# Kernel optimization log

Measured on AMD Instinct MI355X. Metric: run time of the kernel, lower is better.

Reference implementation:

```python
import jax, jax.numpy as jnp
import numpy as np

N_USERS = 60000
N_ITEMS = 40000
N_NODES = N_USERS + N_ITEMS  # 100000
N_EDGES = 3_200_000
EMB_DIM = 64
N_LAYERS = 3
S_TEMP = 1.0  # config['s_temp']
EPS = 1e-16   # torch_geometric.utils.softmax denominator eps


def segment_softmax(logits, seg, num_segments):
    # numerically stable scatter-softmax (PyG softmax semantics)
    m = jax.ops.segment_max(logits, seg, num_segments=num_segments)
    m = jnp.where(jnp.isfinite(m), m, 0.0)  # empty segments -> -inf guard
    e = jnp.exp(logits - m[seg])
    s = jax.ops.segment_sum(e, seg, num_segments=num_segments)
    return e / (s[seg] + EPS)


def setup_inputs() -> dict:
    key = jax.random.key(0)
    k1, k2, k3 = jax.random.split(key, 3)
    # nn.Embedding weight, init normal(std=0.1) for non-NGCF models
    emb = jax.random.normal(k1, (N_NODES, EMB_DIM), dtype=jnp.float32) * 0.1
    edge_index = jax.random.randint(k2, (2, N_EDGES), 0, N_NODES, dtype=jnp.int32)
    edge_attrs = jax.random.normal(k3, (N_EDGES,), dtype=jnp.float32)
    return {"emb": emb, "edge_index": edge_index, "edge_attrs": edge_attrs}


def reference(emb, edge_index, edge_attrs):
    from_, to_ = edge_index[0], edge_index[1]
    logits = edge_attrs / S_TEMP
    incoming = segment_softmax(logits, to_, N_NODES)
    outgoing = segment_softmax(logits, from_, N_NODES)
    norm = jnp.sqrt(incoming * outgoing)  # abl_study == 0 branch

    embs = [emb]
    cur = emb
    for _ in range(N_LAYERS):
        # message: norm * x_j ; aggregate: scatter-add at to_
        msg = norm[:, None] * cur[from_]           # [E, D]
        cur = jax.ops.segment_sum(msg, to_, num_segments=N_NODES)  # [N, D]
        embs.append(cur)

    out = jnp.mean(jnp.stack(embs, axis=0), axis=0)  # lightGCN-style layer mean
    return (emb, out)
```

## Files before the change

kernel.cpp:

```cpp
#include <hip/hip_runtime.h>
#include <math.h>
#include <hip/hip_fp16.h>

#define N_NODES 100000
#define N_EDGES 3200000
#define EPS 1e-16f
#define BSH 8
#define BN 256
#define NBK 391
#define PTT 512
#define PE2 8
#define PTILE (PTT * PE2)
#define GR (PTILE / 16)
#define PBLOCKS ((N_EDGES + PTILE - 1) / PTILE)
#define CAP 9216u
#define NR 4
#define SCALE 8.0f
#define RPT 9

typedef float    f4v __attribute__((ext_vector_type(4)));
typedef float    f2v __attribute__((ext_vector_type(2)));

static __device__ __forceinline__ float4 nt_load_f4(const float4* p) {
    f4v v = __builtin_nontemporal_load((const f4v*)p);
    return make_float4(v.x, v.y, v.z, v.w);
}
static __device__ __forceinline__ int range_of(unsigned f) {
    return (f >= 50000u) ? (f >= 75000u ? 3 : 2) : (f >= 25000u ? 1 : 0);
}

static __device__ __forceinline__ unsigned short f_to_bf(float f) {
    unsigned u = __float_as_uint(f);
    unsigned r = (u + 0x7FFFu + ((u >> 16) & 1u)) >> 16;
    return (unsigned short)r;
}
static __device__ __forceinline__ float slot_w(unsigned s) {
    return __half2float(__ushort_as_half((unsigned short)(s >> 17)));
}
static __device__ __forceinline__ void fma8_fp8(float w, uint2 r, float* a) {
    f2v v0 = __builtin_amdgcn_cvt_pk_f32_fp8((int)r.x, false);
    f2v v1 = __builtin_amdgcn_cvt_pk_f32_fp8((int)r.x, true);
    f2v v2 = __builtin_amdgcn_cvt_pk_f32_fp8((int)r.y, false);
    f2v v3 = __builtin_amdgcn_cvt_pk_f32_fp8((int)r.y, true);
    a[0] = fmaf(w, v0.x, a[0]); a[1] = fmaf(w, v0.y, a[1]);
    a[2] = fmaf(w, v1.x, a[2]); a[3] = fmaf(w, v1.y, a[3]);
    a[4] = fmaf(w, v2.x, a[4]); a[5] = fmaf(w, v2.y, a[5]);
    a[6] = fmaf(w, v3.x, a[6]); a[7] = fmaf(w, v3.y, a[7]);
}
static __device__ __forceinline__ uint4 pack8(const float* a) {
    uint4 o;
    o.x = (unsigned)f_to_bf(a[0]) | ((unsigned)f_to_bf(a[1]) << 16);
    o.y = (unsigned)f_to_bf(a[2]) | ((unsigned)f_to_bf(a[3]) << 16);
    o.z = (unsigned)f_to_bf(a[4]) | ((unsigned)f_to_bf(a[5]) << 16);
    o.w = (unsigned)f_to_bf(a[6]) | ((unsigned)f_to_bf(a[7]) << 16);
    return o;
}
static __device__ __forceinline__ uint2 pack8_fp8(const float* a) {
    int w0 = __builtin_amdgcn_cvt_pk_fp8_f32(a[0], a[1], 0, false);
    w0 = __builtin_amdgcn_cvt_pk_fp8_f32(a[2], a[3], w0, true);
    int w1 = __builtin_amdgcn_cvt_pk_fp8_f32(a[4], a[5], 0, false);
    w1 = __builtin_amdgcn_cvt_pk_fp8_f32(a[6], a[7], w1, true);
    return make_uint2((unsigned)w0, (unsigned)w1);
}
static __device__ __forceinline__ float bfu_to_f(unsigned u, int hi) {
    return __uint_as_float(hi ? (u & 0xFFFF0000u) : (u << 16));
}

__global__ __launch_bounds__(PTT) void partition(
        const int* __restrict__ ei, const float* __restrict__ attr,
        unsigned* __restrict__ pos_t, unsigned* __restrict__ pos_f,
        uint2* __restrict__ bt, unsigned* __restrict__ bf) {
    __shared__ unsigned ht[NBK], hf[NBK];
    __shared__ unsigned hbt[NBK + 1], hbf[NBK + 1];
    __shared__ unsigned dlt[NBK], dlf[NBK];
    __shared__ unsigned short lutT[GR], lutF[GR];
    __shared__ unsigned wsum[8];
    __shared__ unsigned sbtx[PTILE];
    __shared__ unsigned short sbty[PTILE];
    __shared__ unsigned sbf[PTILE];
    const int tid = threadIdx.x;
    const int lane = tid & 63, wid = tid >> 6;
    for (int i = tid; i < NBK; i += PTT) { ht[i] = 0; hf[i] = 0; }
    __syncthreads();
    const int tile = blockIdx.x * PTILE;
    const int tcount = (tile + PTILE < N_EDGES) ? PTILE : (N_EDGES - tile);
    unsigned fv[PE2], tv[PE2];
    unsigned short xh[PE2];
    #pragma unroll
    for (int k = 0; k < PE2; ++k) {
        int e = tile + k * PTT + tid;
        if (e < N_EDGES) {
            fv[k] = (unsigned)__builtin_nontemporal_load(&ei[e]);
            tv[k] = (unsigned)__builtin_nontemporal_load(&ei[N_EDGES + e]);
            xh[k] = __half_as_ushort(__float2half(
                        __expf(__builtin_nontemporal_load(&attr[e]))));
            atomicAdd(&ht[tv[k] >> BSH], 1u);
            atomicAdd(&hf[fv[k] >> BSH], 1u);
        } else {
            tv[k] = 0xFFFFFFFFu;
        }
    }
    __syncthreads();
    unsigned ot = (tid < NBK) ? ht[tid] : 0u;
    unsigned of = (tid < NBK) ? hf[tid] : 0u;
    unsigned own = ot | (of << 16);
    unsigned x = own;
    #pragma unroll
    for (int d = 1; d < 64; d <<= 1) {
        unsigned v = __shfl_up(x, d, 64);
        if (lane >= d) x += v;
    }
    if (lane == 63) wsum[wid] = x;
    __syncthreads();
    unsigned pre = 0;
    for (int w = 0; w < wid; ++w) pre += wsum[w];
    unsigned excl = x + pre - own;
    unsigned et = excl & 0xFFFFu, ef = excl >> 16;
    if (tid < NBK) {
        hbt[tid] = et;
        hbf[tid] = ef;
        unsigned rt = ot ? atomicAdd(&pos_t[tid], ot) : 0u;
        unsigned rf = of ? atomicAdd(&pos_f[tid], of) : 0u;
        dlt[tid] = tid * CAP + rt - et;
        dlf[tid] = tid * CAP + rf - ef;
    }
    if (tid == NBK - 1) { hbt[NBK] = et + ot; hbf[NBK] = ef + of; }
    __syncthreads();
    if (tid < NBK) {
        unsigned b0 = hbt[tid], b1 = hbt[tid + 1];
        for (unsigned g = (b0 + 15u) >> 4; (g << 4) < b1; ++g) lutT[g] = (unsigned short)tid;
        b0 = hbf[tid]; b1 = hbf[tid + 1];
        for (unsigned g = (b0 + 15u) >> 4; (g << 4) < b1; ++g) lutF[g] = (unsigned short)tid;
    }
    for (int i = tid; i < NBK; i += PTT) { ht[i] = hbt[i]; hf[i] = hbf[i]; }
    __syncthreads();
    #pragma unroll
    for (int k = 0; k < PE2; ++k) {
        if (tv[k] != 0xFFFFFFFFu) {
            unsigned p = atomicAdd(&ht[tv[k] >> BSH], 1u);
            sbtx[p] = fv[k] | ((tv[k] & (BN - 1u)) << 17);
            sbty[p] = xh[k];
            unsigned q = atomicAdd(&hf[fv[k] >> BSH], 1u);
            sbf[q] = ((fv[k] & (BN - 1u)) << 16) | (unsigned)xh[k];
        }
    }
    __syncthreads();
    for (int i = tid; i < tcount; i += PTT) {
        unsigned b = lutT[i >> 4];
        while (hbt[b + 1] <= (unsigned)i) ++b;
        unsigned ga = dlt[b] + (unsigned)i;
        if (ga < (b + 1u) * CAP) bt[ga] = make_uint2(sbtx[i], (unsigned)sbty[i]);
    }
    for (int i = tid; i < tcount; i += PTT) {
        unsigned b = lutF[i >> 4];
        while (hbf[b + 1] <= (unsigned)i) ++b;
        unsigned ga = dlf[b] + (unsigned)i;
        if (ga < (b + 1u) * CAP) bf[ga] = sbf[i];
    }
}

__global__ __launch_bounds__(1024) void bucket_build(
        const unsigned* __restrict__ pos_f, const unsigned* __restrict__ bf,
        const unsigned* __restrict__ pos_t, const uint2* __restrict__ bt,
        const float4* __restrict__ emb4, uint2* __restrict__ emb_f8,
        uint2* __restrict__ row2, unsigned* __restrict__ slots,
        float2* __restrict__ sc2) {
    __shared__ float s[BN];
    __shared__ float sto[BN];
    __shared__ unsigned cnt[BN][NR];
    __shared__ unsigned cur[BN][NR];
    __shared__ unsigned wsum[4];
    int b = blockIdx.x, tid = threadIdx.x;
    const int lane = tid & 63, wid = tid >> 6;
    if (tid < BN) {
        s[tid] = 0.f;
        sto[tid] = 0.f;
        #pragma unroll
        for (int r = 0; r < NR; ++r) cnt[tid][r] = 0;
    }
    __syncthreads();
    {
        unsigned fill = pos_f[b]; if (fill > CAP) fill = CAP;
        unsigned lof = b * CAP, hif = lof + fill;
        for (unsigned i = lof + tid; i < hif; i += 1024) {
            unsigned u = __builtin_nontemporal_load(&bf[i]);
            atomicAdd(&s[u >> 16], __half2float(__ushort_as_half((unsigned short)(u & 0xFFFFu))));
        }
    }
    __syncthreads();
    {
        int nl = tid >> 2, part = tid & 3;
        int node = b * BN + nl;
        if (node < N_NODES) {
            float rsv = rsqrtf(s[nl] + EPS) * SCALE;
            size_t rbase = (size_t)node * 16 + part * 4;
            #pragma unroll
            for (int c = 0; c < 2; ++c) {
                float4 v0 = emb4[rbase + c * 2];
                float4 v1 = emb4[rbase + c * 2 + 1];
                float a[8] = {v0.x * rsv, v0.y * rsv, v0.z * rsv, v0.w * rsv,
                              v1.x * rsv, v1.y * rsv, v1.z * rsv, v1.w * rsv};
                emb_f8[(size_t)node * 8 + part * 2 + c] = pack8_fp8(a);
            }
        }
    }
    unsigned fill = pos_t[b]; if (fill > CAP) fill = CAP;
    unsigned lo = b * CAP, hi = lo + fill;
    uint2 rv[RPT];
    #pragma unroll
    for (int j = 0; j < RPT; ++j) {
        unsigned i = lo + tid + (unsigned)j * 1024u;
        if (i < hi) {
            uint2 u = bt[i];
            rv[j] = u;
            unsigned tl = u.x >> 17;
            atomicAdd(&cnt[tl][range_of(u.x & 0x1FFFFu)], 1u);
            atomicAdd(&sto[tl], __half2float(__ushort_as_half((unsigned short)u.y)));
        } else {
            rv[j].x = 0xFFFFFFFFu;
            rv[j].y = 0u;
        }
    }
    __syncthreads();
    unsigned c0 = 0, c1 = 0, c2 = 0, c3 = 0, own = 0;
    if (tid < BN) {
        c0 = cnt[tid][0]; c1 = cnt[tid][1]; c2 = cnt[tid][2]; c3 = cnt[tid][3];
        own = c0 + c1 + c2 + c3;
    }
    unsigned x = own;
    #pragma unroll
    for (int d = 1; d < 64; d <<= 1) {
        unsigned v = __shfl_up(x, d, 64);
        if (lane >= d) x += v;
    }
    if (tid < BN && lane == 63) wsum[wid] = x;
    __syncthreads();
    if (tid < BN) {
        unsigned pre = 0;
        for (int w = 0; w < wid; ++w) pre += wsum[w];
        unsigned base = lo + x + pre - own;
        int node = b * BN + tid;
        if (node < N_NODES) {
            row2[node] = make_uint2(base, base + own);
            float rt = rsqrtf(sto[tid] + EPS);
            sc2[node] = make_float2(rt * (1.0f / SCALE), rt * rsqrtf(s[tid] + EPS));
        }
        cur[tid][0] = base;
        cur[tid][1] = base + c0;
        cur[tid][2] = base + c0 + c1;
        cur[tid][3] = base + c0 + c1 + c2;
    }
    __syncthreads();
    #pragma unroll
    for (int j = 0; j < RPT; ++j) {
        if (rv[j].x != 0xFFFFFFFFu) {
            unsigned tl = rv[j].x >> 17;
            unsigned f = rv[j].x & 0x1FFFFu;
            unsigned p = atomicAdd(&cur[tl][range_of(f)], 1u);
            slots[p] = f | (rv[j].y << 17);
        }
    }
}

#define GATHER_CORE8(TABLE)                                                       \
    float a[8] = {0, 0, 0, 0, 0, 0, 0, 0};                                        \
    float bacc[8] = {0, 0, 0, 0, 0, 0, 0, 0};                                     \
    unsigned k = beg;                                                             \
    for (; k + 8 <= end; k += 8) {                                                \
        unsigned s0 = slots[k], s1 = slots[k + 1], s2 = slots[k + 2], s3 = slots[k + 3]; \
        unsigned s4 = slots[k + 4], s5 = slots[k + 5], s6 = slots[k + 6], s7 = slots[k + 7]; \
        uint2 r0 = TABLE[(size_t)(s0 & 0x1FFFFu) * 8 + lane];                     \
        uint2 r1 = TABLE[(size_t)(s1 & 0x1FFFFu) * 8 + lane];                     \
        uint2 r2 = TABLE[(size_t)(s2 & 0x1FFFFu) * 8 + lane];                     \
        uint2 r3 = TABLE[(size_t)(s3 & 0x1FFFFu) * 8 + lane];                     \
        uint2 r4 = TABLE[(size_t)(s4 & 0x1FFFFu) * 8 + lane];                     \
        uint2 r5 = TABLE[(size_t)(s5 & 0x1FFFFu) * 8 + lane];                     \
        uint2 r6 = TABLE[(size_t)(s6 & 0x1FFFFu) * 8 + lane];                     \
        uint2 r7 = TABLE[(size_t)(s7 & 0x1FFFFu) * 8 + lane];                     \
        fma8_fp8(slot_w(s0), r0, a);    fma8_fp8(slot_w(s1), r1, bacc);           \
        fma8_fp8(slot_w(s2), r2, a);    fma8_fp8(slot_w(s3), r3, bacc);           \
        fma8_fp8(slot_w(s4), r4, a);    fma8_fp8(slot_w(s5), r5, bacc);           \
        fma8_fp8(slot_w(s6), r6, a);    fma8_fp8(slot_w(s7), r7, bacc);           \
    }                                                                             \
    for (; k < end; ++k) {                                                        \
        unsigned s = slots[k];                                                    \
        uint2 r = TABLE[(size_t)(s & 0x1FFFFu) * 8 + lane];                       \
        fma8_fp8(slot_w(s), r, a);                                                \
    }                                                                             \
    _Pragma("unroll")                                                             \
    for (int j = 0; j < 8; ++j) a[j] += bacc[j];

__global__ void prop1(const uint2* __restrict__ row2, const unsigned* __restrict__ slots,
                      const uint2* __restrict__ emb_f8, const float2* __restrict__ sc2,
                      uint2* __restrict__ T1f8, uint4* __restrict__ T1bf,
                      const float4* __restrict__ emb4, float4* __restrict__ out_emb4) {
    int node = blockIdx.x * 32 + (threadIdx.x >> 3);
    int lane = threadIdx.x & 7;
    if (node < N_NODES) {
        uint2 rp = row2[node];
        unsigned beg = rp.x, end = rp.y;
        GATHER_CORE8(emb_f8)
        float2 sc = sc2[node];
        float own[8], tab[8];
        #pragma unroll
        for (int j = 0; j < 8; ++j) { own[j] = a[j] * sc.x; tab[j] = a[j] * sc.y; }
        size_t o = (size_t)node * 8 + lane;
        T1bf[o] = pack8(own);
        T1f8[o] = pack8_fp8(tab);
    }
    const int total = N_NODES * 16;
    const int stride = ((N_NODES * 8 + 255) / 256) * 256;
    for (int i = blockIdx.x * 256 + threadIdx.x; i < total; i += stride) {
        out_emb4[i] = nt_load_f4(&emb4[i]);
    }
}

__global__ void prop2(const uint2* __restrict__ row2, const unsigned* __restrict__ slots,
                      const uint2* __restrict__ T1f8, const float2* __restrict__ sc2,
                      uint2* __restrict__ T2f8, uint4* __restrict__ T2bf) {
    int node = blockIdx.x * 32 + (threadIdx.x >> 3);
    int lane = threadIdx.x & 7;
    if (node >= N_NODES) return;
    uint2 rp = row2[node];
    unsigned beg = rp.x, end = rp.y;
    GATHER_CORE8(T1f8)
    float2 sc = sc2[node];
    float own[8], tab[8];
    #pragma unroll
    for (int j = 0; j < 8; ++j) { own[j] = a[j] * sc.x; tab[j] = a[j] * sc.y; }
    size_t o = (size_t)node * 8 + lane;
    T2bf[o] = pack8(own);
    T2f8[o] = pack8_fp8(tab);
}

__global__ void prop3(const uint2* __restrict__ row2, const unsigned* __restrict__ slots,
                      const uint2* __restrict__ T2f8, const float2* __restrict__ sc2,
                      const uint4* __restrict__ T1bf, const uint4* __restrict__ T2bf,
                      const float4* __restrict__ emb4, float4* __restrict__ acc) {
    int node = blockIdx.x * 32 + (threadIdx.x >> 3);
    int lane = threadIdx.x & 7;
    if (node >= N_NODES) return;
    uint2 rp = row2[node];
    unsigned beg = rp.x, end = rp.y;
    GATHER_CORE8(T2f8)
    float osc = sc2[node].x;
    size_t o = (size_t)node * 8 + lane;
    uint4 t1 = T1bf[o];
    uint4 t2 = T2bf[o];
    unsigned tw1[4] = {t1.x, t1.y, t1.z, t1.w};
    unsigned tw2[4] = {t2.x, t2.y, t2.z, t2.w};
    size_t o4 = (size_t)node * 16 + lane * 2;
    float4 e0 = emb4[o4], e1 = emb4[o4 + 1];
    float e[8] = {e0.x, e0.y, e0.z, e0.w, e1.x, e1.y, e1.z, e1.w};
    float r[8];
    #pragma unroll
    for (int j = 0; j < 8; ++j) {
        float l1v = bfu_to_f(tw1[j >> 1], j & 1);
        float l2v = bfu_to_f(tw2[j >> 1], j & 1);
        r[j] = (e[j] + l1v + l2v + a[j] * osc) * 0.25f;
    }
    acc[o4]     = make_float4(r[0], r[1], r[2], r[3]);
    acc[o4 + 1] = make_float4(r[4], r[5], r[6], r[7]);
}

extern "C" void kernel_launch(void* const* d_in, const int* in_sizes, int n_in,
                              void* d_out, int out_size, void* d_ws, size_t ws_size,
                              hipStream_t stream) {
    const float* emb = (const float*)d_in[0];
    const int* ei = (const int*)d_in[1];
    const float* attr = (const float*)d_in[2];

    float* out_emb = (float*)d_out;
    float* out_acc = out_emb + (size_t)N_NODES * 64;

    char* ws = (char*)d_ws;
    size_t off = 0;
    auto alloc = [&](size_t bytes) -> void* {
        void* p = ws + off;
        off += (bytes + 255) & ~(size_t)255;
        return p;
    };
    unsigned* pos_t   = (unsigned*)alloc((size_t)NBK * 4);
    unsigned* pos_f   = (unsigned*)alloc((size_t)NBK * 4);
    size_t zero_bytes = off;
    uint2*    row2    = (uint2*)   alloc((size_t)N_NODES * 8);
    float2*   sc2     = (float2*)  alloc((size_t)N_NODES * 8);
    uint2* bt         = (uint2*)   alloc((size_t)NBK * CAP * 8);
    unsigned* bfa     = (unsigned*)alloc((size_t)NBK * CAP * 4);
    unsigned* slots   = bfa;
    uint2* emb_f8     = (uint2*)   alloc((size_t)N_NODES * 64);
    uint2* T1f8       = (uint2*)   alloc((size_t)N_NODES * 64);
    uint4* T1bf       = (uint4*)   alloc((size_t)N_NODES * 128);
    uint2* T2f8 = (uint2*)bt;
    uint4* T2bf = (uint4*)((char*)bt + (size_t)N_NODES * 64);
    (void)ws_size;

    hipMemsetAsync(d_ws, 0, zero_bytes, stream);

    partition<<<PBLOCKS, PTT, 0, stream>>>(ei, attr, pos_t, pos_f, bt, bfa);
    bucket_build<<<NBK, 1024, 0, stream>>>(pos_f, bfa, pos_t, bt,
                                           (const float4*)emb, emb_f8,
                                           row2, slots, sc2);

    const int pgrid = (N_NODES * 8 + 255) / 256;
    prop1<<<pgrid, 256, 0, stream>>>(row2, slots, emb_f8, sc2, T1f8, T1bf,
                                     (const float4*)emb, (float4*)out_emb);
    prop2<<<pgrid, 256, 0, stream>>>(row2, slots, T1f8, sc2, T2f8, T2bf);
    prop3<<<pgrid, 256, 0, stream>>>(row2, slots, T2f8, sc2, T1bf, T2bf,
                                     (const float4*)emb, (float4*)out_acc);
}
```

Measured before the change: 247.7 us.

## Split bucket_build into from-sum and to-CSR kernels; separate load and atomic loops

Splits the fused bucket_build kernel into two launches. bucket_sum_f computes per-source softmax denominators and the fp8 embedding table. bucket_csr_t builds the CSR slots by re-reading the bt bucket in a second pass instead of holding 9 uint2 entries per thread in registers. In partition, the global loads are hoisted into their own loop ahead of the LDS histogram atomics so more loads can be in flight. This trades an extra launch, an extra global read of bt, and a small s_from_inv buffer for lower register pressure and possibly better occupancy and load overlap.

```diff
diff --git a/kernel.cpp b/kernel.cpp
--- a/kernel.cpp
+++ b/kernel.cpp
@@ -16,7 +16,6 @@
 #define CAP 9216u
 #define NR 4
 #define SCALE 8.0f
-#define RPT 9
 
 typedef float    f4v __attribute__((ext_vector_type(4)));
 typedef float    f2v __attribute__((ext_vector_type(2)));
@@ -94,10 +93,15 @@
             tv[k] = (unsigned)__builtin_nontemporal_load(&ei[N_EDGES + e]);
             xh[k] = __half_as_ushort(__float2half(
                         __expf(__builtin_nontemporal_load(&attr[e]))));
+        } else {
+            tv[k] = 0xFFFFFFFFu;
+        }
+    }
+    #pragma unroll
+    for (int k = 0; k < PE2; ++k) {
+        if (tv[k] != 0xFFFFFFFFu) {
             atomicAdd(&ht[tv[k] >> BSH], 1u);
             atomicAdd(&hf[fv[k] >> BSH], 1u);
-        } else {
-            tv[k] = 0xFFFFFFFFu;
         }
     }
     __syncthreads();
@@ -159,13 +163,46 @@
     }
 }
 
-__global__ __launch_bounds__(1024) void bucket_build(
+__global__ __launch_bounds__(1024) void bucket_sum_f(
         const unsigned* __restrict__ pos_f, const unsigned* __restrict__ bf,
+        float* __restrict__ s_from_inv,
+        const float4* __restrict__ emb4, uint2* __restrict__ emb_f8) {
+    __shared__ float s[BN];
+    int b = blockIdx.x, tid = threadIdx.x;
+    if (tid < BN) s[tid] = 0.f;
+    __syncthreads();
+    unsigned fill = pos_f[b]; if (fill > CAP) fill = CAP;
+    unsigned lo = b * CAP, hi = lo + fill;
+    for (unsigned i = lo + tid; i < hi; i += 1024) {
+        unsigned u = __builtin_nontemporal_load(&bf[i]);
+        atomicAdd(&s[u >> 16], __half2float(__ushort_as_half((unsigned short)(u & 0xFFFFu))));
+    }
+    __syncthreads();
+    if (tid < BN) {
+        int node = b * BN + tid;
+        if (node < N_NODES) s_from_inv[node] = rsqrtf(s[tid] + EPS);
+    }
+    int nl = tid >> 2, part = tid & 3;
+    int node = b * BN + nl;
+    if (node < N_NODES) {
+        float rsv = rsqrtf(s[nl] + EPS) * SCALE;
+        size_t rbase = (size_t)node * 16 + part * 4;
+        #pragma unroll
+        for (int c = 0; c < 2; ++c) {
+            float4 v0 = emb4[rbase + c * 2];
+            float4 v1 = emb4[rbase + c * 2 + 1];
+            float a[8] = {v0.x * rsv, v0.y * rsv, v0.z * rsv, v0.w * rsv,
+                          v1.x * rsv, v1.y * rsv, v1.z * rsv, v1.w * rsv};
+            emb_f8[(size_t)node * 8 + part * 2 + c] = pack8_fp8(a);
+        }
+    }
+}
+
+__global__ __launch_bounds__(1024) void bucket_csr_t(
         const unsigned* __restrict__ pos_t, const uint2* __restrict__ bt,
-        const float4* __restrict__ emb4, uint2* __restrict__ emb_f8,
+        const float* __restrict__ s_from_inv,
         uint2* __restrict__ row2, unsigned* __restrict__ slots,
         float2* __restrict__ sc2) {
-    __shared__ float s[BN];
     __shared__ float sto[BN];
     __shared__ unsigned cnt[BN][NR];
     __shared__ unsigned cur[BN][NR];
@@ -173,53 +210,18 @@
     int b = blockIdx.x, tid = threadIdx.x;
     const int lane = tid & 63, wid = tid >> 6;
     if (tid < BN) {
-        s[tid] = 0.f;
         sto[tid] = 0.f;
         #pragma unroll
         for (int r = 0; r < NR; ++r) cnt[tid][r] = 0;
     }
     __syncthreads();
-    {
-        unsigned fill = pos_f[b]; if (fill > CAP) fill = CAP;
-        unsigned lof = b * CAP, hif = lof + fill;
-        for (unsigned i = lof + tid; i < hif; i += 1024) {
-            unsigned u = __builtin_nontemporal_load(&bf[i]);
-            atomicAdd(&s[u >> 16], __half2float(__ushort_as_half((unsigned short)(u & 0xFFFFu))));
-        }
-    }
-    __syncthreads();
-    {
-        int nl = tid >> 2, part = tid & 3;
-        int node = b * BN + nl;
-        if (node < N_NODES) {
-            float rsv = rsqrtf(s[nl] + EPS) * SCALE;
-            size_t rbase = (size_t)node * 16 + part * 4;
-            #pragma unroll
-            for (int c = 0; c < 2; ++c) {
-                float4 v0 = emb4[rbase + c * 2];
-                float4 v1 = emb4[rbase + c * 2 + 1];
-                float a[8] = {v0.x * rsv, v0.y * rsv, v0.z * rsv, v0.w * rsv,
-                              v1.x * rsv, v1.y * rsv, v1.z * rsv, v1.w * rsv};
-                emb_f8[(size_t)node * 8 + part * 2 + c] = pack8_fp8(a);
-            }
-        }
-    }
     unsigned fill = pos_t[b]; if (fill > CAP) fill = CAP;
     unsigned lo = b * CAP, hi = lo + fill;
-    uint2 rv[RPT];
-    #pragma unroll
-    for (int j = 0; j < RPT; ++j) {
-        unsigned i = lo + tid + (unsigned)j * 1024u;
-        if (i < hi) {
-            uint2 u = bt[i];
-            rv[j] = u;
-            unsigned tl = u.x >> 17;
-            atomicAdd(&cnt[tl][range_of(u.x & 0x1FFFFu)], 1u);
-            atomicAdd(&sto[tl], __half2float(__ushort_as_half((unsigned short)u.y)));
-        } else {
-            rv[j].x = 0xFFFFFFFFu;
-            rv[j].y = 0u;
-        }
+    for (unsigned i = lo + tid; i < hi; i += 1024) {
+        uint2 u = bt[i];
+        unsigned tl = u.x >> 17;
+        atomicAdd(&cnt[tl][range_of(u.x & 0x1FFFFu)], 1u);
+        atomicAdd(&sto[tl], __half2float(__ushort_as_half((unsigned short)u.y)));
     }
     __syncthreads();
     unsigned c0 = 0, c1 = 0, c2 = 0, c3 = 0, own = 0;
@@ -243,7 +245,7 @@
         if (node < N_NODES) {
             row2[node] = make_uint2(base, base + own);
             float rt = rsqrtf(sto[tid] + EPS);
-            sc2[node] = make_float2(rt * (1.0f / SCALE), rt * rsqrtf(s[tid] + EPS));
+            sc2[node] = make_float2(rt * (1.0f / SCALE), rt * s_from_inv[node]);
         }
         cur[tid][0] = base;
         cur[tid][1] = base + c0;
@@ -251,14 +253,12 @@
         cur[tid][3] = base + c0 + c1 + c2;
     }
     __syncthreads();
-    #pragma unroll
-    for (int j = 0; j < RPT; ++j) {
-        if (rv[j].x != 0xFFFFFFFFu) {
-            unsigned tl = rv[j].x >> 17;
-            unsigned f = rv[j].x & 0x1FFFFu;
-            unsigned p = atomicAdd(&cur[tl][range_of(f)], 1u);
-            slots[p] = f | (rv[j].y << 17);
-        }
+    for (unsigned i = lo + tid; i < hi; i += 1024) {
+        uint2 u = bt[i];
+        unsigned tl = u.x >> 17;
+        unsigned f = u.x & 0x1FFFFu;
+        unsigned p = atomicAdd(&cur[tl][range_of(f)], 1u);
+        slots[p] = f | (u.y << 17);
     }
 }
 
@@ -384,6 +384,7 @@
     unsigned* pos_f   = (unsigned*)alloc((size_t)NBK * 4);
     size_t zero_bytes = off;
     uint2*    row2    = (uint2*)   alloc((size_t)N_NODES * 8);
+    float*  s_from_inv= (float*)   alloc((size_t)N_NODES * 4);
     float2*   sc2     = (float2*)  alloc((size_t)N_NODES * 8);
     uint2* bt         = (uint2*)   alloc((size_t)NBK * CAP * 8);
     unsigned* bfa     = (unsigned*)alloc((size_t)NBK * CAP * 4);
@@ -398,9 +399,9 @@
     hipMemsetAsync(d_ws, 0, zero_bytes, stream);
 
     partition<<<PBLOCKS, PTT, 0, stream>>>(ei, attr, pos_t, pos_f, bt, bfa);
-    bucket_build<<<NBK, 1024, 0, stream>>>(pos_f, bfa, pos_t, bt,
-                                           (const float4*)emb, emb_f8,
-                                           row2, slots, sc2);
+    bucket_sum_f<<<NBK, 1024, 0, stream>>>(pos_f, bfa, s_from_inv,
+                                           (const float4*)emb, emb_f8);
+    bucket_csr_t<<<NBK, 1024, 0, stream>>>(pos_t, bt, s_from_inv, row2, slots, sc2);
 
     const int pgrid = (N_NODES * 8 + 255) / 256;
     prop1<<<pgrid, 256, 0, stream>>>(row2, slots, emb_f8, sc2, T1f8, T1bf,
```

New measurement: 253.3 us. 2.2% more time.
